# Kernel tuning notes

Hardware: AMD Instinct MI355X
Metric: run time of the kernel (lower is better)

## Reference

```python
import jax, jax.numpy as jnp
import numpy as np

EMBED_DIM = 1024
HIDDEN = 128
N_QUERY = 65536
N_PROTO = 512


def setup_inputs() -> dict:
    key = jax.random.key(0)
    k1, k2, k3, k4, k5, k6, k7 = jax.random.split(key, 7)
    d2 = EMBED_DIM * 2
    lim1 = 1.0 / np.sqrt(d2)
    lim2 = 1.0 / np.sqrt(HIDDEN)
    return {
        "query_features": jax.random.normal(k1, (N_QUERY, EMBED_DIM), dtype=jnp.float32),
        "prototypes": jax.random.normal(k2, (N_PROTO, EMBED_DIM), dtype=jnp.float32),
        "distances": jax.random.uniform(k3, (N_QUERY, N_PROTO), dtype=jnp.float32),
        "W1": jax.random.uniform(k4, (d2, HIDDEN), minval=-lim1, maxval=lim1, dtype=jnp.float32),
        "b1": jax.random.uniform(k5, (HIDDEN,), minval=-lim1, maxval=lim1, dtype=jnp.float32),
        "W2": jax.random.uniform(k6, (HIDDEN, 1), minval=-lim2, maxval=lim2, dtype=jnp.float32),
        "b2": jax.random.uniform(k7, (1,), minval=-lim2, maxval=lim2, dtype=jnp.float32),
    }


def reference(query_features, prototypes, distances, W1, b1, W2, b2):
    # Batched version of the per-query loop: argmin -> gather -> concat -> MLP.
    idx = jnp.argmin(distances, axis=1)                      # [N_QUERY]
    closest = prototypes[idx]                                # [N_QUERY, D]
    combined = jnp.concatenate([query_features, closest], axis=-1)  # [N_QUERY, 2D]
    h = jax.nn.relu(combined @ W1 + b1)                      # [N_QUERY, 128]
    out = jax.nn.sigmoid(h @ W2 + b2)                        # [N_QUERY, 1]
    return jnp.squeeze(out, axis=-1)                         # [N_QUERY]
```

## Files before the change

kernel.cpp:

```cpp
#include <hip/hip_runtime.h>
#include <hip/hip_bf16.h>
#include <math.h>

#define EMBED 1024
#define HIDDEN 128
#define NPROTO 512
#define LDA 72

typedef short bf16x8 __attribute__((ext_vector_type(8)));
typedef float f32x4 __attribute__((ext_vector_type(4)));

__device__ __forceinline__ unsigned short f2bf(float x) {
    unsigned u = __builtin_bit_cast(unsigned, x);
    unsigned r = u + 0x7FFFu + ((u >> 16) & 1u);
    return (unsigned short)(r >> 16);
}

__global__ __launch_bounds__(256) void prep_kernel(
    const float* __restrict__ prototypes,
    const float* __restrict__ W1,
    float* __restrict__ proto_h,
    unsigned short* __restrict__ w1t)
{
    int b = blockIdx.x;
    int t = threadIdx.x;
    if (b < 256) {
        int ph = t >> 7, h = t & 127;
        int p = b * 2 + ph;
        const float* pr = prototypes + (size_t)p * EMBED;
        const float* w  = W1 + (size_t)EMBED * HIDDEN + h;
        float acc = 0.f;
        for (int k = 0; k < EMBED; k += 8) {
            #pragma unroll
            for (int j = 0; j < 8; ++j)
                acc += pr[k + j] * w[(size_t)(k + j) * HIDDEN];
        }
        proto_h[(size_t)p * HIDDEN + h] = acc;
    } else {
        int s = (b - 256) * 256 + t;
        int n = s & 127;
        int k0 = (s >> 7) * 8;
        bf16x8 v;
        #pragma unroll
        for (int j = 0; j < 8; ++j)
            v[j] = (short)f2bf(W1[(size_t)(k0 + j) * HIDDEN + n]);
        *(bf16x8*)(w1t + (size_t)n * EMBED + k0) = v;
    }
}

__global__ __launch_bounds__(256, 3) void main_kernel(
    const float* __restrict__ qf,
    const float* __restrict__ dist,
    const float* __restrict__ b1,
    const float* __restrict__ W2,
    const float* __restrict__ b2,
    const float* __restrict__ proto_h,
    const unsigned short* __restrict__ w1t,
    float* __restrict__ out)
{
    __shared__ unsigned short a_lds[2][128 * LDA];
    __shared__ int s_idx[128];
    __shared__ float s_red[128][2];

    int t = threadIdx.x;
    int wave = t >> 6, lane = t & 63;
    int q0 = blockIdx.x * 128;

    int sm = t >> 3;
    int sk = (t & 7) * 8;

    float4 pre[4][2];
    {
        const float* base = qf + (size_t)q0 * EMBED;
        #pragma unroll
        for (int i = 0; i < 4; ++i) {
            const float* src = base + (size_t)(sm + i * 32) * EMBED + sk;
            pre[i][0] = *(const float4*)src;
            pre[i][1] = *(const float4*)(src + 4);
        }
    }

    for (int i = 0; i < 32; i += 4) {
        float4 v0[4], v1[4];
        #pragma unroll
        for (int j = 0; j < 4; ++j) {
            const float* dr = dist + (size_t)(q0 + wave * 32 + i + j) * NPROTO;
            v0[j] = ((const float4*)dr)[lane];
            v1[j] = ((const float4*)dr)[lane + 64];
        }
        #pragma unroll
        for (int j = 0; j < 4; ++j) {
            float bv = v0[j].x; int bi = lane * 4;
            if (v0[j].y < bv) { bv = v0[j].y; bi = lane * 4 + 1; }
            if (v0[j].z < bv) { bv = v0[j].z; bi = lane * 4 + 2; }
            if (v0[j].w < bv) { bv = v0[j].w; bi = lane * 4 + 3; }
            int c = 256 + lane * 4;
            if (v1[j].x < bv) { bv = v1[j].x; bi = c; }
            if (v1[j].y < bv) { bv = v1[j].y; bi = c + 1; }
            if (v1[j].z < bv) { bv = v1[j].z; bi = c + 2; }
            if (v1[j].w < bv) { bv = v1[j].w; bi = c + 3; }
            #pragma unroll
            for (int s = 1; s < 64; s <<= 1) {
                float ov = __shfl_xor(bv, s);
                int   oi = __shfl_xor(bi, s);
                if (ov < bv || (ov == bv && oi < bi)) { bv = ov; bi = oi; }
            }
            if (lane == 0) s_idx[wave * 32 + i + j] = bi;
        }
    }

    #pragma unroll
    for (int i = 0; i < 4; ++i) {
        bf16x8 pk;
        pk[0] = (short)f2bf(pre[i][0].x); pk[1] = (short)f2bf(pre[i][0].y);
        pk[2] = (short)f2bf(pre[i][0].z); pk[3] = (short)f2bf(pre[i][0].w);
        pk[4] = (short)f2bf(pre[i][1].x); pk[5] = (short)f2bf(pre[i][1].y);
        pk[6] = (short)f2bf(pre[i][1].z); pk[7] = (short)f2bf(pre[i][1].w);
        *(bf16x8*)(&a_lds[0][(sm + i * 32) * LDA + sk]) = pk;
    }
    __syncthreads();

    int wave_m = wave >> 1, wave_n = wave & 1;
    int quad = lane >> 4, tid16 = lane & 15;
    f32x4 acc[4][4];
    #pragma unroll
    for (int mi = 0; mi < 4; ++mi)
        #pragma unroll
        for (int ni = 0; ni < 4; ++ni)
            acc[mi][ni] = (f32x4){0.f, 0.f, 0.f, 0.f};

    for (int kt = 0; kt < EMBED; kt += 64) {
        int cur = (kt >> 6) & 1;
        bool more = (kt + 64) < EMBED;

        bf16x8 bfr[2][4];
        #pragma unroll
        for (int ks = 0; ks < 2; ++ks)
            #pragma unroll
            for (int ni = 0; ni < 4; ++ni)
                bfr[ks][ni] = *(const bf16x8*)(
                    w1t + (size_t)(wave_n * 64 + ni * 16 + tid16) * EMBED
                        + kt + ks * 32 + quad * 8);

        if (more) {
            const float* base = qf + (size_t)q0 * EMBED + kt + 64;
            #pragma unroll
            for (int i = 0; i < 4; ++i) {
                const float* src = base + (size_t)(sm + i * 32) * EMBED + sk;
                pre[i][0] = *(const float4*)src;
                pre[i][1] = *(const float4*)(src + 4);
            }
        }

        #pragma unroll
        for (int ks = 0; ks < 2; ++ks) {
            int kk = ks * 32 + quad * 8;
            bf16x8 af[4];
            #pragma unroll
            for (int mi = 0; mi < 4; ++mi)
                af[mi] = *(bf16x8*)(&a_lds[cur][(wave_m * 64 + mi * 16 + tid16) * LDA + kk]);
            #pragma unroll
            for (int mi = 0; mi < 4; ++mi)
                #pragma unroll
                for (int ni = 0; ni < 4; ++ni)
                    acc[mi][ni] = __builtin_amdgcn_mfma_f32_16x16x32_bf16(
                        af[mi], bfr[ks][ni], acc[mi][ni], 0, 0, 0);
        }

        if (more) {
            #pragma unroll
            for (int i = 0; i < 4; ++i) {
                bf16x8 pk;
                pk[0] = (short)f2bf(pre[i][0].x); pk[1] = (short)f2bf(pre[i][0].y);
                pk[2] = (short)f2bf(pre[i][0].z); pk[3] = (short)f2bf(pre[i][0].w);
                pk[4] = (short)f2bf(pre[i][1].x); pk[5] = (short)f2bf(pre[i][1].y);
                pk[6] = (short)f2bf(pre[i][1].z); pk[7] = (short)f2bf(pre[i][1].w);
                *(bf16x8*)(&a_lds[cur ^ 1][(sm + i * 32) * LDA + sk]) = pk;
            }
        }
        __syncthreads();
    }

    float b1v[4], w2v[4];
    #pragma unroll
    for (int ni = 0; ni < 4; ++ni) {
        int n = wave_n * 64 + ni * 16 + tid16;
        b1v[ni] = b1[n];
        w2v[ni] = W2[n];
    }
    #pragma unroll
    for (int mi = 0; mi < 4; ++mi) {
        #pragma unroll
        for (int r = 0; r < 4; ++r) {
            int m = wave_m * 64 + mi * 16 + quad * 4 + r;
            const float* ph = proto_h + (size_t)s_idx[m] * HIDDEN;
            float sum = 0.f;
            #pragma unroll
            for (int ni = 0; ni < 4; ++ni) {
                int n = wave_n * 64 + ni * 16 + tid16;
                float v = acc[mi][ni][r] + b1v[ni] + ph[n];
                sum += fmaxf(v, 0.f) * w2v[ni];
            }
            #pragma unroll
            for (int s = 1; s < 16; s <<= 1) sum += __shfl_xor(sum, s);
            if (tid16 == 0) s_red[m][wave_n] = sum;
        }
    }
    __syncthreads();
    if (t < 128) {
        float s = s_red[t][0] + s_red[t][1] + b2[0];
        out[q0 + t] = 1.f / (1.f + expf(-s));
    }
}

extern "C" void kernel_launch(void* const* d_in, const int* in_sizes, int n_in,
                              void* d_out, int out_size, void* d_ws, size_t ws_size,
                              hipStream_t stream) {
    const float* qf    = (const float*)d_in[0];
    const float* proto = (const float*)d_in[1];
    const float* dist  = (const float*)d_in[2];
    const float* W1    = (const float*)d_in[3];
    const float* b1    = (const float*)d_in[4];
    const float* W2    = (const float*)d_in[5];
    const float* b2    = (const float*)d_in[6];
    float* out = (float*)d_out;

    float* proto_h = (float*)d_ws;
    unsigned short* w1t = (unsigned short*)((char*)d_ws + 512 * 128 * 4);

    prep_kernel<<<320, 256, 0, stream>>>(proto, W1, proto_h, w1t);

    int nq = in_sizes[0] / EMBED;
    main_kernel<<<nq / 128, 256, 0, stream>>>(qf, dist, b1, W2, b2, proto_h, w1t, out);
}
```

Baseline: 500.5 us.

## Drop LDS staging; each wave loads A fragments directly and owns full N

Restructures the main GEMM so each wave handles 32 query rows across all 128 hidden units. A fragments are loaded from global memory straight into registers in MFMA layout and converted to bf16 there, with no shared-memory tile. This removes LDS traffic and all block-level __syncthreads, and the final reduction is written per wave instead of combined across waves. The cost is higher register pressure (launch bounds go from 3 to 2 waves) and scattered 32-byte global loads of A, with W1 fragments re-read per wave.

```diff
diff --git a/kernel.cpp b/kernel.cpp
--- a/kernel.cpp
+++ b/kernel.cpp
@@ -1,11 +1,9 @@
 #include <hip/hip_runtime.h>
-#include <hip/hip_bf16.h>
 #include <math.h>
 
 #define EMBED 1024
 #define HIDDEN 128
 #define NPROTO 512
-#define LDA 72
 
 typedef short bf16x8 __attribute__((ext_vector_type(8)));
 typedef float f32x4 __attribute__((ext_vector_type(4)));
@@ -48,7 +46,7 @@
     }
 }
 
-__global__ __launch_bounds__(256, 3) void main_kernel(
+__global__ __launch_bounds__(256, 2) void main_kernel(
     const float* __restrict__ qf,
     const float* __restrict__ dist,
     const float* __restrict__ b1,
@@ -58,33 +56,31 @@
     const unsigned short* __restrict__ w1t,
     float* __restrict__ out)
 {
-    __shared__ unsigned short a_lds[2][128 * LDA];
-    __shared__ int s_idx[128];
-    __shared__ float s_red[128][2];
-
-    int t = threadIdx.x;
-    int wave = t >> 6, lane = t & 63;
-    int q0 = blockIdx.x * 128;
-
-    int sm = t >> 3;
-    int sk = (t & 7) * 8;
-
-    float4 pre[4][2];
-    {
-        const float* base = qf + (size_t)q0 * EMBED;
-        #pragma unroll
-        for (int i = 0; i < 4; ++i) {
-            const float* src = base + (size_t)(sm + i * 32) * EMBED + sk;
-            pre[i][0] = *(const float4*)src;
-            pre[i][1] = *(const float4*)(src + 4);
-        }
+    __shared__ int s_idx[4][32];
+
+    const int t = threadIdx.x;
+    const int wave = t >> 6, lane = t & 63;
+    const int quad = lane >> 4, tid16 = lane & 15;
+    const int q0 = blockIdx.x * 128 + wave * 32;
+
+    const float* abase = qf + (size_t)(q0 + tid16) * EMBED + quad * 8;
+    const unsigned short* bbase = w1t + (size_t)tid16 * EMBED + quad * 8;
+
+    float4 aA[2][2], aB[2][2];
+    #pragma unroll
+    for (int mi = 0; mi < 2; ++mi) {
+        const float* p = abase + (size_t)(mi * 16) * EMBED;
+        aA[mi][0] = *(const float4*)(p);
+        aA[mi][1] = *(const float4*)(p + 4);
+        aB[mi][0] = *(const float4*)(p + 32);
+        aB[mi][1] = *(const float4*)(p + 36);
     }
 
     for (int i = 0; i < 32; i += 4) {
         float4 v0[4], v1[4];
         #pragma unroll
         for (int j = 0; j < 4; ++j) {
-            const float* dr = dist + (size_t)(q0 + wave * 32 + i + j) * NPROTO;
+            const float* dr = dist + (size_t)(q0 + i + j) * NPROTO;
             v0[j] = ((const float4*)dr)[lane];
             v1[j] = ((const float4*)dr)[lane + 64];
         }
@@ -105,111 +101,100 @@
                 int   oi = __shfl_xor(bi, s);
                 if (ov < bv || (ov == bv && oi < bi)) { bv = ov; bi = oi; }
             }
-            if (lane == 0) s_idx[wave * 32 + i + j] = bi;
-        }
-    }
-
-    #pragma unroll
-    for (int i = 0; i < 4; ++i) {
-        bf16x8 pk;
-        pk[0] = (short)f2bf(pre[i][0].x); pk[1] = (short)f2bf(pre[i][0].y);
-        pk[2] = (short)f2bf(pre[i][0].z); pk[3] = (short)f2bf(pre[i][0].w);
-        pk[4] = (short)f2bf(pre[i][1].x); pk[5] = (short)f2bf(pre[i][1].y);
-        pk[6] = (short)f2bf(pre[i][1].z); pk[7] = (short)f2bf(pre[i][1].w);
-        *(bf16x8*)(&a_lds[0][(sm + i * 32) * LDA + sk]) = pk;
-    }
-    __syncthreads();
-
-    int wave_m = wave >> 1, wave_n = wave & 1;
-    int quad = lane >> 4, tid16 = lane & 15;
-    f32x4 acc[4][4];
-    #pragma unroll
-    for (int mi = 0; mi < 4; ++mi)
-        #pragma unroll
-        for (int ni = 0; ni < 4; ++ni)
+            if (lane == 0) s_idx[wave][i + j] = bi;
+        }
+    }
+
+    f32x4 acc[2][8];
+    #pragma unroll
+    for (int mi = 0; mi < 2; ++mi)
+        #pragma unroll
+        for (int ni = 0; ni < 8; ++ni)
             acc[mi][ni] = (f32x4){0.f, 0.f, 0.f, 0.f};
 
-    for (int kt = 0; kt < EMBED; kt += 64) {
-        int cur = (kt >> 6) & 1;
-        bool more = (kt + 64) < EMBED;
-
-        bf16x8 bfr[2][4];
-        #pragma unroll
-        for (int ks = 0; ks < 2; ++ks)
-            #pragma unroll
-            for (int ni = 0; ni < 4; ++ni)
-                bfr[ks][ni] = *(const bf16x8*)(
-                    w1t + (size_t)(wave_n * 64 + ni * 16 + tid16) * EMBED
-                        + kt + ks * 32 + quad * 8);
-
-        if (more) {
-            const float* base = qf + (size_t)q0 * EMBED + kt + 64;
-            #pragma unroll
-            for (int i = 0; i < 4; ++i) {
-                const float* src = base + (size_t)(sm + i * 32) * EMBED + sk;
-                pre[i][0] = *(const float4*)src;
-                pre[i][1] = *(const float4*)(src + 4);
-            }
-        }
-
-        #pragma unroll
-        for (int ks = 0; ks < 2; ++ks) {
-            int kk = ks * 32 + quad * 8;
-            bf16x8 af[4];
-            #pragma unroll
-            for (int mi = 0; mi < 4; ++mi)
-                af[mi] = *(bf16x8*)(&a_lds[cur][(wave_m * 64 + mi * 16 + tid16) * LDA + kk]);
-            #pragma unroll
-            for (int mi = 0; mi < 4; ++mi)
+#define LOAD_A(dst, kk)                                              \
+    do {                                                             \
+        _Pragma("unroll")                                            \
+        for (int mi = 0; mi < 2; ++mi) {                             \
+            const float* p = abase + (size_t)(mi * 16) * EMBED + (kk) * 32; \
+            dst[mi][0] = *(const float4*)(p);                        \
+            dst[mi][1] = *(const float4*)(p + 4);                    \
+        }                                                            \
+    } while (0)
+
+#define CVT_A(af, src)                                               \
+    do {                                                             \
+        _Pragma("unroll")                                            \
+        for (int mi = 0; mi < 2; ++mi) {                             \
+            af[mi][0] = (short)f2bf(src[mi][0].x);                   \
+            af[mi][1] = (short)f2bf(src[mi][0].y);                   \
+            af[mi][2] = (short)f2bf(src[mi][0].z);                   \
+            af[mi][3] = (short)f2bf(src[mi][0].w);                   \
+            af[mi][4] = (short)f2bf(src[mi][1].x);                   \
+            af[mi][5] = (short)f2bf(src[mi][1].y);                   \
+            af[mi][6] = (short)f2bf(src[mi][1].z);                   \
+            af[mi][7] = (short)f2bf(src[mi][1].w);                   \
+        }                                                            \
+    } while (0)
+
+    for (int k = 0; k < 32; k += 2) {
+        {
+            bf16x8 bfr[8];
+            #pragma unroll
+            for (int ni = 0; ni < 8; ++ni)
+                bfr[ni] = *(const bf16x8*)(bbase + (size_t)(ni * 16) * EMBED + k * 32);
+            bf16x8 af[2];
+            CVT_A(af, aA);
+            if (k + 2 < 32) LOAD_A(aA, k + 2);
+            #pragma unroll
+            for (int mi = 0; mi < 2; ++mi)
                 #pragma unroll
-                for (int ni = 0; ni < 4; ++ni)
+                for (int ni = 0; ni < 8; ++ni)
                     acc[mi][ni] = __builtin_amdgcn_mfma_f32_16x16x32_bf16(
-                        af[mi], bfr[ks][ni], acc[mi][ni], 0, 0, 0);
-        }
-
-        if (more) {
-            #pragma unroll
-            for (int i = 0; i < 4; ++i) {
-                bf16x8 pk;
-                pk[0] = (short)f2bf(pre[i][0].x); pk[1] = (short)f2bf(pre[i][0].y);
-                pk[2] = (short)f2bf(pre[i][0].z); pk[3] = (short)f2bf(pre[i][0].w);
-                pk[4] = (short)f2bf(pre[i][1].x); pk[5] = (short)f2bf(pre[i][1].y);
-                pk[6] = (short)f2bf(pre[i][1].z); pk[7] = (short)f2bf(pre[i][1].w);
-                *(bf16x8*)(&a_lds[cur ^ 1][(sm + i * 32) * LDA + sk]) = pk;
-            }
-        }
-        __syncthreads();
-    }
-
-    float b1v[4], w2v[4];
-    #pragma unroll
-    for (int ni = 0; ni < 4; ++ni) {
-        int n = wave_n * 64 + ni * 16 + tid16;
-        b1v[ni] = b1[n];
-        w2v[ni] = W2[n];
-    }
-    #pragma unroll
-    for (int mi = 0; mi < 4; ++mi) {
+                        af[mi], bfr[ni], acc[mi][ni], 0, 0, 0);
+        }
+        {
+            bf16x8 bfr[8];
+            #pragma unroll
+            for (int ni = 0; ni < 8; ++ni)
+                bfr[ni] = *(const bf16x8*)(bbase + (size_t)(ni * 16) * EMBED + (k + 1) * 32);
+            bf16x8 af[2];
+            CVT_A(af, aB);
+            if (k + 3 < 32) LOAD_A(aB, k + 3);
+            #pragma unroll
+            for (int mi = 0; mi < 2; ++mi)
+                #pragma unroll
+                for (int ni = 0; ni < 8; ++ni)
+                    acc[mi][ni] = __builtin_amdgcn_mfma_f32_16x16x32_bf16(
+                        af[mi], bfr[ni], acc[mi][ni], 0, 0, 0);
+        }
+    }
+#undef LOAD_A
+#undef CVT_A
+
+    float b1v[8], w2v[8];
+    #pragma unroll
+    for (int ni = 0; ni < 8; ++ni) {
+        b1v[ni] = b1[ni * 16 + tid16];
+        w2v[ni] = W2[ni * 16 + tid16];
+    }
+    const float b2v = b2[0];
+    #pragma unroll
+    for (int mi = 0; mi < 2; ++mi) {
         #pragma unroll
         for (int r = 0; r < 4; ++r) {
-            int m = wave_m * 64 + mi * 16 + quad * 4 + r;
-            const float* ph = proto_h + (size_t)s_idx[m] * HIDDEN;
+            int m = mi * 16 + quad * 4 + r;
+            const float* ph = proto_h + (size_t)s_idx[wave][m] * HIDDEN + tid16;
             float sum = 0.f;
             #pragma unroll
-            for (int ni = 0; ni < 4; ++ni) {
-                int n = wave_n * 64 + ni * 16 + tid16;
-                float v = acc[mi][ni][r] + b1v[ni] + ph[n];
+            for (int ni = 0; ni < 8; ++ni) {
+                float v = acc[mi][ni][r] + b1v[ni] + ph[ni * 16];
                 sum += fmaxf(v, 0.f) * w2v[ni];
             }
             #pragma unroll
             for (int s = 1; s < 16; s <<= 1) sum += __shfl_xor(sum, s);
-            if (tid16 == 0) s_red[m][wave_n] = sum;
-        }
-    }
-    __syncthreads();
-    if (t < 128) {
-        float s = s_red[t][0] + s_red[t][1] + b2[0];
-        out[q0 + t] = 1.f / (1.f + expf(-s));
+            if (tid16 == 0) out[q0 + m] = 1.f / (1.f + expf(-(sum + b2v)));
+        }
     }
 }
 
```

Result: slower. 529.4 us (+5.8%).
